# Kernel optimization log

Measured on AMD Instinct MI355X. Metric: run time of the kernel, lower is better.

Reference implementation:

```python
import jax, jax.numpy as jnp
import numpy as np

N_SITES = 100000
DIM = 128
KSIZE = 7  # 7^3 = 343 offsets
GRID = 160


def _build_sparse_structure(seed=0):
    """Sample N_SITES unique voxels in a GRID^3 volume and build the
    depthwise-conv kernel map: neighbor_idx[i, k] = index of site at
    coords[i] + offset[k], or N_SITES (sentinel -> zero row) if absent."""
    rng = np.random.default_rng(seed)
    lin = rng.choice(GRID ** 3, size=N_SITES, replace=False)
    coords = np.stack(np.unravel_index(lin, (GRID, GRID, GRID)), axis=1).astype(np.int64)  # [N,3]
    lookup = np.full(GRID ** 3, N_SITES, dtype=np.int32)
    lookup[lin] = np.arange(N_SITES, dtype=np.int32)
    r = KSIZE // 2
    offs = np.stack(np.meshgrid(*([np.arange(-r, r + 1)] * 3), indexing="ij"), axis=-1).reshape(-1, 3)  # [343,3]
    K = offs.shape[0]
    neighbor_idx = np.full((N_SITES, K), N_SITES, dtype=np.int32)
    for k in range(K):
        nb = coords + offs[k]
        ok = np.all((nb >= 0) & (nb < GRID), axis=1)
        nb_lin = (nb[ok, 0] * GRID + nb[ok, 1]) * GRID + nb[ok, 2]
        neighbor_idx[ok, k] = lookup[nb_lin]
    return neighbor_idx


def setup_inputs() -> dict:
    key = jax.random.key(0)
    ks = jax.random.split(key, 12)
    neighbor_idx = jnp.asarray(_build_sparse_structure(0))
    d, h = DIM, 4 * DIM
    K = KSIZE ** 3
    return {
        "feats": jax.random.normal(ks[0], (N_SITES, d), jnp.float32),
        "neighbor_idx": neighbor_idx,
        "dw_w": jax.random.normal(ks[1], (K, d), jnp.float32) * 0.05,
        "dw_b": jax.random.normal(ks[2], (d,), jnp.float32) * 0.02,
        "ln_g": 1.0 + 0.1 * jax.random.normal(ks[3], (d,), jnp.float32),
        "ln_b": 0.02 * jax.random.normal(ks[4], (d,), jnp.float32),
        "w1": jax.random.normal(ks[5], (d, h), jnp.float32) * (1.0 / np.sqrt(d)),
        "b1": 0.02 * jax.random.normal(ks[6], (h,), jnp.float32),
        "grn_g": 0.1 * jax.random.normal(ks[7], (1, h), jnp.float32),
        "grn_b": 0.02 * jax.random.normal(ks[8], (1, h), jnp.float32),
        "w2": jax.random.normal(ks[9], (h, d), jnp.float32) * (1.0 / np.sqrt(h)),
        "b2": 0.02 * jax.random.normal(ks[10], (d,), jnp.float32),
    }


def reference(feats, neighbor_idx, dw_w, dw_b, ln_g, ln_b, w1, b1, grn_g, grn_b, w2, b2):
    eps = 1e-6
    n, d = feats.shape
    # --- sparse depthwise conv: gather-multiply-accumulate over kernel offsets ---
    f_pad = jnp.concatenate([feats, jnp.zeros((1, d), feats.dtype)], axis=0)  # sentinel row

    def step(acc, xs):
        idx_k, w_k = xs  # idx_k: [N], w_k: [dim]
        return acc + f_pad[idx_k] * w_k, None

    x, _ = jax.lax.scan(step, jnp.zeros_like(feats), (neighbor_idx.T, dw_w))
    x = x + dw_b
    # --- LayerNorm over channels ---
    mu = jnp.mean(x, axis=-1, keepdims=True)
    var = jnp.var(x, axis=-1, keepdims=True)
    x = (x - mu) / jnp.sqrt(var + eps) * ln_g + ln_b
    # --- pwconv1 -> GELU (exact, matching torch default) ---
    x = jax.nn.gelu(x @ w1 + b1, approximate=False)  # [N, 4*dim]
    # --- GRN: L2 norm over all sites (dim=0), per channel ---
    gx = jnp.sqrt(jnp.sum(x * x, axis=0, keepdims=True))  # [1, 4*dim]
    nx = gx / (jnp.mean(gx, axis=-1, keepdims=True) + eps)
    x = grn_g * (x * nx) + grn_b + x
    # --- pwconv2 + residual (drop_path identity in eval) ---
    x = x @ w2 + b2
    return feats + x
```

## Files before the change

kernel.cpp:

```cpp
#include <hip/hip_runtime.h>

typedef unsigned short u16;
typedef unsigned int u32;
typedef __attribute__((ext_vector_type(8))) short bf16x8;
typedef __attribute__((ext_vector_type(4))) float f32x4;

__device__ __forceinline__ u16 f2bf(float f) {
    u32 u = __float_as_uint(f);
    return (u16)((u + 0x7FFFu + ((u >> 16) & 1u)) >> 16);
}

__device__ __forceinline__ float fast_gelu(float x) {
    const float t = x * x;
    const float y2 = x * __builtin_fmaf(0.0713548214f, t, 1.5957691216057308f);
    const float u = __expf(fminf(y2, 80.f));
    return x * u * __builtin_amdgcn_rcpf(u + 1.f);
}

__device__ __forceinline__ void gload_lds16(const u16* g, u16* l) {
    __builtin_amdgcn_global_load_lds(
        (const __attribute__((address_space(1))) void*)g,
        (__attribute__((address_space(3))) void*)l, 16, 0, 0);
}

__global__ __launch_bounds__(256) void cast_feats_k(
    const float* __restrict__ src, u16* __restrict__ dst, int n4)
{
    const int e = blockIdx.x * 256 + threadIdx.x;
    if (e >= n4) return;
    const float4 v = *(const float4*)(src + (size_t)e * 4);
    uint2 o;
    o.x = (u32)f2bf(v.x) | ((u32)f2bf(v.y) << 16);
    o.y = (u32)f2bf(v.z) | ((u32)f2bf(v.w) << 16);
    *(uint2*)(dst + (size_t)e * 4) = o;
}

__global__ __launch_bounds__(256) void dwln_k(
    const u16* __restrict__ featsb, const int* __restrict__ nb,
    const u16* __restrict__ dwwb, const float* __restrict__ dw_b,
    const float* __restrict__ ln_g, const float* __restrict__ ln_b,
    u16* __restrict__ xln, int nsites)
{
    __shared__ int lists[8][348];
    const int w = threadIdx.x >> 6;
    const int lane = threadIdx.x & 63;
    const int s0 = blockIdx.x * 8 + w * 2;
    if (s0 >= nsites) return;
    const bool two = (s0 + 1) < nsites;
    const int* rowA = nb + (size_t)s0 * 343;
    const int* rowB = nb + (size_t)(two ? s0 + 1 : s0) * 343;
    int idxA[6], idxB[6];
    #pragma unroll
    for (int j = 0; j < 5; ++j) {
        idxA[j] = rowA[lane + j * 64];
        const int vb = rowB[lane + j * 64];
        idxB[j] = two ? vb : nsites;
    }
    idxA[5] = (lane < 23) ? rowA[320 + lane] : nsites;
    idxB[5] = (two && lane < 23) ? rowB[320 + lane] : nsites;
    int cA = 0, cB = 0;
    #pragma unroll
    for (int i = 0; i < 6; ++i) {
        cA += (idxA[i] < nsites) ? 1 : 0;
        cB += (idxB[i] < nsites) ? 1 : 0;
    }
    const int packed = cA | (cB << 16);
    int pre = packed;
    #pragma unroll
    for (int off = 1; off < 64; off <<= 1) {
        const int v = __shfl_up(pre, off, 64);
        if (lane >= off) pre += v;
    }
    const int tot = __shfl(pre, 63, 64);
    const int cntA = tot & 0xFFFF, cntB = tot >> 16;
    pre -= packed;
    int pA = pre & 0xFFFF, pB = pre >> 16;
    #pragma unroll
    for (int i = 0; i < 6; ++i) {
        const int k = (i < 5) ? (lane + i * 64) : (320 + lane);
        if (idxA[i] < nsites) lists[w * 2][pA++] = idxA[i] | (k << 17);
        if (idxB[i] < nsites) lists[w * 2 + 1][pB++] = idxB[i] | (k << 17);
    }
    float xA0 = 0.f, xA1 = 0.f, xB0 = 0.f, xB1 = 0.f;
    const int mx = (cntA > cntB) ? cntA : cntB;
    for (int base = 0; base < mx; base += 4) {
        u32 fa[4], wa[4], fb[4], wb[4];
        #pragma unroll
        for (int i = 0; i < 4; ++i) {
            if (base + i < cntA) {
                const int p = lists[w * 2][base + i];
                fa[i] = *(const u32*)(featsb + (size_t)(p & 0x1FFFF) * 128 + lane * 2);
                wa[i] = *(const u32*)(dwwb + (size_t)(p >> 17) * 128 + lane * 2);
            } else { fa[i] = 0u; wa[i] = 0u; }
            if (base + i < cntB) {
                const int p = lists[w * 2 + 1][base + i];
                fb[i] = *(const u32*)(featsb + (size_t)(p & 0x1FFFF) * 128 + lane * 2);
                wb[i] = *(const u32*)(dwwb + (size_t)(p >> 17) * 128 + lane * 2);
            } else { fb[i] = 0u; wb[i] = 0u; }
        }
        #pragma unroll
        for (int i = 0; i < 4; ++i) {
            xA0 += __uint_as_float(fa[i] << 16) * __uint_as_float(wa[i] << 16);
            xA1 += __uint_as_float(fa[i] & 0xFFFF0000u) * __uint_as_float(wa[i] & 0xFFFF0000u);
            xB0 += __uint_as_float(fb[i] << 16) * __uint_as_float(wb[i] << 16);
            xB1 += __uint_as_float(fb[i] & 0xFFFF0000u) * __uint_as_float(wb[i] & 0xFFFF0000u);
        }
    }
    const float2 bv = *(const float2*)(dw_b + lane * 2);
    const float2 gv = *(const float2*)(ln_g + lane * 2);
    const float2 lbv = *(const float2*)(ln_b + lane * 2);
    #pragma unroll
    for (int sidx = 0; sidx < 2; ++sidx) {
        if (sidx == 1 && !two) break;
        float a0 = (sidx == 0) ? xA0 : xB0;
        float a1 = (sidx == 0) ? xA1 : xB1;
        a0 += bv.x; a1 += bv.y;
        float s = a0 + a1, ss = a0 * a0 + a1 * a1;
        #pragma unroll
        for (int off = 32; off > 0; off >>= 1) {
            s += __shfl_xor(s, off, 64);
            ss += __shfl_xor(ss, off, 64);
        }
        const float mean = s * (1.f / 128.f);
        const float var = ss * (1.f / 128.f) - mean * mean;
        const float rstd = rsqrtf(fmaxf(var, 0.f) + 1e-6f);
        const float y0 = (a0 - mean) * rstd * gv.x + lbv.x;
        const float y1 = (a1 - mean) * rstd * gv.y + lbv.y;
        *(u32*)(xln + (size_t)(s0 + sidx) * 128 + lane * 2) =
            (u32)f2bf(y0) | ((u32)f2bf(y1) << 16);
    }
}

__global__ __launch_bounds__(256) void transpose_w1_k(
    const float* __restrict__ w1, u16* __restrict__ w1t)
{
    const int e = blockIdx.x * 256 + threadIdx.x;
    const int n = e >> 7, k = e & 127;
    w1t[e] = f2bf(w1[k * 512 + n]);
}

__global__ __launch_bounds__(256, 4) void gemm1_k(
    const u16* __restrict__ xln, const u16* __restrict__ w1t,
    const float* __restrict__ b1, u16* __restrict__ h,
    float* __restrict__ gx_sq, int nsites)
{
    __shared__ u16 xb[64 * 128];
    __shared__ float s_red[128];
    const int t = threadIdx.x;
    const int n0 = blockIdx.x * 128;
    const int m0 = blockIdx.y * 64;
    const int lane = t & 63;
    const int w = t >> 6;
    const int wn = w * 32;
    const int l15 = lane & 15, quad = lane >> 4;
    if (t < 128) s_red[t] = 0.f;
    #pragma unroll
    for (int i = 0; i < 4; ++i) {
        const int r = w * 16 + i * 4 + (lane >> 4);
        const int c = (lane & 15) ^ (r & 15);
        gload_lds16(xln + (size_t)(m0 + r) * 128 + c * 8,
                    &xb[(w * 16 + i * 4) * 128]);
    }
    f32x4 acc[2][4];
    #pragma unroll
    for (int i = 0; i < 2; ++i)
        #pragma unroll
        for (int j = 0; j < 4; ++j) acc[i][j] = f32x4{0.f, 0.f, 0.f, 0.f};
    const u16* a_base = w1t + (size_t)(n0 + wn + l15) * 128 + quad * 8;
    bf16x8 aC[2];
    #pragma unroll
    for (int nt = 0; nt < 2; ++nt) aC[nt] = *(const bf16x8*)(a_base + (size_t)nt * 16 * 128);
    asm volatile("s_waitcnt vmcnt(0)" ::: "memory");
    __syncthreads();
    #pragma unroll
    for (int ks = 0; ks < 4; ++ks) {
        bf16x8 aN[2];
        if (ks < 3) {
            #pragma unroll
            for (int nt = 0; nt < 2; ++nt)
                aN[nt] = *(const bf16x8*)(a_base + (size_t)nt * 16 * 128 + (ks + 1) * 32);
        }
        bf16x8 b[4];
        #pragma unroll
        for (int mt = 0; mt < 4; ++mt) {
            const int r = mt * 16 + l15;
            b[mt] = *(const bf16x8*)(&xb[r * 128 + (((ks * 4 + quad) ^ l15) << 3)]);
        }
        #pragma unroll
        for (int nt = 0; nt < 2; ++nt)
            #pragma unroll
            for (int mt = 0; mt < 4; ++mt)
                acc[nt][mt] = __builtin_amdgcn_mfma_f32_16x16x32_bf16(aC[nt], b[mt], acc[nt][mt], 0, 0, 0);
        if (ks < 3) {
            #pragma unroll
            for (int nt = 0; nt < 2; ++nt) aC[nt] = aN[nt];
        }
    }
    float ssl[2][4] = {{0.f,0.f,0.f,0.f},{0.f,0.f,0.f,0.f}};
    #pragma unroll
    for (int nt = 0; nt < 2; ++nt) {
        const int chb = n0 + wn + nt * 16 + quad * 4;
        const float4 b1v = *(const float4*)(b1 + chb);
        #pragma unroll
        for (int mt = 0; mt < 4; ++mt) {
            const int site = m0 + mt * 16 + l15;
            if (site < nsites) {
                float v[4];
                #pragma unroll
                for (int rg = 0; rg < 4; ++rg) {
                    v[rg] = fast_gelu(acc[nt][mt][rg] + ((const float*)&b1v)[rg]);
                    ssl[nt][rg] += v[rg] * v[rg];
                }
                uint2 o;
                o.x = (u32)f2bf(v[0]) | ((u32)f2bf(v[1]) << 16);
                o.y = (u32)f2bf(v[2]) | ((u32)f2bf(v[3]) << 16);
                *(uint2*)(h + (size_t)site * 512 + chb) = o;
            }
        }
    }
    #pragma unroll
    for (int nt = 0; nt < 2; ++nt)
        #pragma unroll
        for (int rg = 0; rg < 4; ++rg) {
            float v = ssl[nt][rg];
            v += __shfl_xor(v, 1, 64);
            v += __shfl_xor(v, 2, 64);
            v += __shfl_xor(v, 4, 64);
            v += __shfl_xor(v, 8, 64);
            if (l15 == 0) atomicAdd(&s_red[wn + nt * 16 + quad * 4 + rg], v);
        }
    __syncthreads();
    if (t < 128) atomicAdd(&gx_sq[n0 + t], s_red[t]);
}

__global__ __launch_bounds__(256) void beff_k(
    const float* __restrict__ grn_b, const float* __restrict__ w2,
    float* __restrict__ b_eff)
{
    __shared__ float red[256];
    const int t = threadIdx.x;
    const int dc = t & 127, part = t >> 7;
    const int c0 = blockIdx.x * 64 + part * 32;
    float p = 0.f;
    #pragma unroll 8
    for (int i = 0; i < 32; ++i) {
        const int c = c0 + i;
        p += grn_b[c] * w2[(size_t)c * 128 + dc];
    }
    red[t] = p;
    __syncthreads();
    if (t < 128) atomicAdd(&b_eff[t], red[t] + red[t + 128]);
}

__global__ __launch_bounds__(512) void grn_scale_k(
    const float* __restrict__ gx_sq, const float* __restrict__ grn_g,
    float* __restrict__ scale)
{
    __shared__ float red[512];
    const int t = threadIdx.x;
    const float g = sqrtf(gx_sq[t]);
    red[t] = g;
    __syncthreads();
    #pragma unroll
    for (int off = 256; off > 0; off >>= 1) {
        if (t < off) red[t] += red[t + off];
        __syncthreads();
    }
    const float mean = red[0] * (1.f / 512.f);
    scale[t] = grn_g[t] * (g / (mean + 1e-6f)) + 1.f;
}

__global__ __launch_bounds__(256) void w2t_k(
    const float* __restrict__ scale, const float* __restrict__ w2,
    u16* __restrict__ w2t)
{
    const int e = blockIdx.x * 256 + threadIdx.x;
    const int c = e & 511, dc = e >> 9;
    w2t[e] = f2bf(scale[c] * w2[(size_t)c * 128 + dc]);
}

__global__ __launch_bounds__(256, 4) void gemm2_k(
    const u16* __restrict__ h, const u16* __restrict__ w2t,
    const float* __restrict__ b_eff, const float* __restrict__ b2,
    const float* __restrict__ feats,
    float* __restrict__ out, int nsites)
{
    __shared__ u16 hb[2][64 * 128];
    const int t = threadIdx.x;
    const int m0 = blockIdx.x * 64;
    const int lane = t & 63;
    const int w = t >> 6;
    const int wn = w * 32;
    const int l15 = lane & 15, quad = lane >> 4;
    const int r_st = w * 16 + (lane >> 4) * 4 ? 0 : 0;
    f32x4 acc[2][4];
    #pragma unroll
    for (int i = 0; i < 2; ++i)
        #pragma unroll
        for (int j = 0; j < 4; ++j) acc[i][j] = f32x4{0.f, 0.f, 0.f, 0.f};
    const u16* a_base = w2t + (size_t)(wn + l15) * 512 + quad * 8;

    #define STAGE2(bsel, tc)                                                     \
        {                                                                        \
            _Pragma("unroll")                                                    \
            for (int i_ = 0; i_ < 4; ++i_) {                                     \
                const int r_ = w * 16 + i_ * 4 + (lane >> 4);                    \
                const int c_ = (lane & 15) ^ (r_ & 15);                          \
                gload_lds16(h + (size_t)(m0 + r_) * 512 + (tc) * 128 + c_ * 8,   \
                            &hb[bsel][(w * 16 + i_ * 4) * 128]);                 \
            }                                                                    \
        }

    STAGE2(0, 0)
    bf16x8 aC[2];
    #pragma unroll
    for (int nt = 0; nt < 2; ++nt) aC[nt] = *(const bf16x8*)(a_base + (size_t)nt * 16 * 512);
    asm volatile("s_waitcnt vmcnt(0)" ::: "memory");
    __syncthreads();
    #pragma unroll
    for (int tch = 0; tch < 4; ++tch) {
        const int cur = tch & 1;
        if (tch < 3) STAGE2(cur ^ 1, tch + 1)
        #pragma unroll
        for (int ks = 0; ks < 4; ++ks) {
            const int ksg = tch * 4 + ks;
            bf16x8 aN[2];
            if (ksg < 15) {
                #pragma unroll
                for (int nt = 0; nt < 2; ++nt)
                    aN[nt] = *(const bf16x8*)(a_base + (size_t)nt * 16 * 512 + (ksg + 1) * 32);
            }
            bf16x8 b[4];
            #pragma unroll
            for (int mt = 0; mt < 4; ++mt) {
                const int r = mt * 16 + l15;
                b[mt] = *(const bf16x8*)(&hb[cur][r * 128 + (((ks * 4 + quad) ^ l15) << 3)]);
            }
            #pragma unroll
            for (int nt = 0; nt < 2; ++nt)
                #pragma unroll
                for (int mt = 0; mt < 4; ++mt)
                    acc[nt][mt] = __builtin_amdgcn_mfma_f32_16x16x32_bf16(aC[nt], b[mt], acc[nt][mt], 0, 0, 0);
            if (ksg < 15) {
                #pragma unroll
                for (int nt = 0; nt < 2; ++nt) aC[nt] = aN[nt];
            }
        }
        if (tch < 3) {
            asm volatile("s_waitcnt vmcnt(0)" ::: "memory");
            __syncthreads();
        }
    }
    #undef STAGE2
    #pragma unroll
    for (int nt = 0; nt < 2; ++nt) {
        const int chb = wn + nt * 16 + quad * 4;
        const float4 bev = *(const float4*)(b_eff + chb);
        const float4 b2v = *(const float4*)(b2 + chb);
        #pragma unroll
        for (int mt = 0; mt < 4; ++mt) {
            const int site = m0 + mt * 16 + l15;
            if (site < nsites) {
                const float4 fv = *(const float4*)(feats + (size_t)site * 128 + chb);
                float4 o;
                o.x = acc[nt][mt][0] + bev.x + b2v.x + fv.x;
                o.y = acc[nt][mt][1] + bev.y + b2v.y + fv.y;
                o.z = acc[nt][mt][2] + bev.z + b2v.z + fv.z;
                o.w = acc[nt][mt][3] + bev.w + b2v.w + fv.w;
                *(float4*)(out + (size_t)site * 128 + chb) = o;
            }
        }
    }
}

extern "C" void kernel_launch(void* const* d_in, const int* in_sizes, int n_in,
                              void* d_out, int out_size, void* d_ws, size_t ws_size,
                              hipStream_t stream) {
    const float* feats = (const float*)d_in[0];
    const int* nb      = (const int*)d_in[1];
    const float* dw_w  = (const float*)d_in[2];
    const float* dw_b  = (const float*)d_in[3];
    const float* ln_g  = (const float*)d_in[4];
    const float* ln_b  = (const float*)d_in[5];
    const float* w1    = (const float*)d_in[6];
    const float* b1    = (const float*)d_in[7];
    const float* grn_g = (const float*)d_in[8];
    const float* grn_b = (const float*)d_in[9];
    const float* w2    = (const float*)d_in[10];
    const float* b2    = (const float*)d_in[11];
    float* out = (float*)d_out;
    const int nsites = in_sizes[0] / 128;

    char* ws = (char*)d_ws;
    size_t off = 0;
    u16* xln   = (u16*)(ws + off);  off += (((size_t)(nsites + 128) * 128 * 2) + 255) & ~(size_t)255;
    u16* h     = (u16*)(ws + off);  off += (((size_t)(nsites + 128) * 512 * 2) + 255) & ~(size_t)255;
    u16* featsb= (u16*)(ws + off);  off += (((size_t)nsites * 128 * 2) + 255) & ~(size_t)255;
    u16* dwwb  = (u16*)(ws + off);  off += 343 * 128 * 2 + 128;
    u16* w1t   = (u16*)(ws + off);  off += 512 * 128 * 2;
    u16* w2t   = (u16*)(ws + off);  off += 128 * 512 * 2;
    float* gx_sq = (float*)(ws + off); off += 512 * 4;
    float* scale = (float*)(ws + off); off += 512 * 4;
    float* b_eff = (float*)(ws + off); off += 128 * 4;

    hipMemsetAsync(gx_sq, 0, 512 * sizeof(float), stream);
    hipMemsetAsync(b_eff, 0, 128 * sizeof(float), stream);
    const int nfeat4 = nsites * 32;
    cast_feats_k<<<(nfeat4 + 255) / 256, 256, 0, stream>>>(feats, featsb, nfeat4);
    const int ndww4 = 343 * 32;
    cast_feats_k<<<(ndww4 + 255) / 256, 256, 0, stream>>>(dw_w, dwwb, ndww4);
    transpose_w1_k<<<256, 256, 0, stream>>>(w1, w1t);
    beff_k<<<8, 256, 0, stream>>>(grn_b, w2, b_eff);
    dwln_k<<<(nsites + 7) / 8, 256, 0, stream>>>(featsb, nb, dwwb, dw_b, ln_g, ln_b, xln, nsites);
    const int m1blocks = (nsites + 63) / 64;
    gemm1_k<<<dim3(4, m1blocks), 256, 0, stream>>>(xln, w1t, b1, h, gx_sq, nsites);
    grn_scale_k<<<1, 512, 0, stream>>>(gx_sq, grn_g, scale);
    w2t_k<<<256, 256, 0, stream>>>(scale, w2, w2t);
    const int m2blocks = (nsites + 63) / 64;
    gemm2_k<<<m2blocks, 256, 0, stream>>>(h, w2t, b_eff, b2, feats, out, nsites);
}
```

Baseline: 411.0 us.

## Gather fp32 features directly in depthwise conv, drop bf16 cast kernels

```diff
diff --git a/kernel.cpp b/kernel.cpp
--- a/kernel.cpp
+++ b/kernel.cpp
@@ -23,112 +23,73 @@
         (__attribute__((address_space(3))) void*)l, 16, 0, 0);
 }
 
-__global__ __launch_bounds__(256) void cast_feats_k(
-    const float* __restrict__ src, u16* __restrict__ dst, int n4)
-{
-    const int e = blockIdx.x * 256 + threadIdx.x;
-    if (e >= n4) return;
-    const float4 v = *(const float4*)(src + (size_t)e * 4);
-    uint2 o;
-    o.x = (u32)f2bf(v.x) | ((u32)f2bf(v.y) << 16);
-    o.y = (u32)f2bf(v.z) | ((u32)f2bf(v.w) << 16);
-    *(uint2*)(dst + (size_t)e * 4) = o;
-}
-
 __global__ __launch_bounds__(256) void dwln_k(
-    const u16* __restrict__ featsb, const int* __restrict__ nb,
-    const u16* __restrict__ dwwb, const float* __restrict__ dw_b,
+    const float* __restrict__ feats, const int* __restrict__ nb,
+    const float* __restrict__ dw_w, const float* __restrict__ dw_b,
     const float* __restrict__ ln_g, const float* __restrict__ ln_b,
     u16* __restrict__ xln, int nsites)
 {
-    __shared__ int lists[8][348];
+    __shared__ int lists[4][344];
     const int w = threadIdx.x >> 6;
     const int lane = threadIdx.x & 63;
-    const int s0 = blockIdx.x * 8 + w * 2;
-    if (s0 >= nsites) return;
-    const bool two = (s0 + 1) < nsites;
-    const int* rowA = nb + (size_t)s0 * 343;
-    const int* rowB = nb + (size_t)(two ? s0 + 1 : s0) * 343;
-    int idxA[6], idxB[6];
-    #pragma unroll
-    for (int j = 0; j < 5; ++j) {
-        idxA[j] = rowA[lane + j * 64];
-        const int vb = rowB[lane + j * 64];
-        idxB[j] = two ? vb : nsites;
-    }
-    idxA[5] = (lane < 23) ? rowA[320 + lane] : nsites;
-    idxB[5] = (two && lane < 23) ? rowB[320 + lane] : nsites;
-    int cA = 0, cB = 0;
-    #pragma unroll
-    for (int i = 0; i < 6; ++i) {
-        cA += (idxA[i] < nsites) ? 1 : 0;
-        cB += (idxB[i] < nsites) ? 1 : 0;
-    }
-    const int packed = cA | (cB << 16);
-    int pre = packed;
+    const int s = blockIdx.x * 4 + w;
+    if (s >= nsites) return;
+    const int* row = nb + (size_t)s * 343;
+    int idx[6];
+    #pragma unroll
+    for (int j = 0; j < 5; ++j) idx[j] = row[lane + j * 64];
+    idx[5] = (lane < 23) ? row[320 + lane] : nsites;
+    int c = 0;
+    #pragma unroll
+    for (int i = 0; i < 6; ++i) c += (idx[i] < nsites) ? 1 : 0;
+    int pre = c;
     #pragma unroll
     for (int off = 1; off < 64; off <<= 1) {
         const int v = __shfl_up(pre, off, 64);
         if (lane >= off) pre += v;
     }
-    const int tot = __shfl(pre, 63, 64);
-    const int cntA = tot & 0xFFFF, cntB = tot >> 16;
-    pre -= packed;
-    int pA = pre & 0xFFFF, pB = pre >> 16;
+    const int cnt = __shfl(pre, 63, 64);
+    pre -= c;
+    int p = pre;
     #pragma unroll
     for (int i = 0; i < 6; ++i) {
         const int k = (i < 5) ? (lane + i * 64) : (320 + lane);
-        if (idxA[i] < nsites) lists[w * 2][pA++] = idxA[i] | (k << 17);
-        if (idxB[i] < nsites) lists[w * 2 + 1][pB++] = idxB[i] | (k << 17);
-    }
-    float xA0 = 0.f, xA1 = 0.f, xB0 = 0.f, xB1 = 0.f;
-    const int mx = (cntA > cntB) ? cntA : cntB;
-    for (int base = 0; base < mx; base += 4) {
-        u32 fa[4], wa[4], fb[4], wb[4];
-        #pragma unroll
-        for (int i = 0; i < 4; ++i) {
-            if (base + i < cntA) {
-                const int p = lists[w * 2][base + i];
-                fa[i] = *(const u32*)(featsb + (size_t)(p & 0x1FFFF) * 128 + lane * 2);
-                wa[i] = *(const u32*)(dwwb + (size_t)(p >> 17) * 128 + lane * 2);
-            } else { fa[i] = 0u; wa[i] = 0u; }
-            if (base + i < cntB) {
-                const int p = lists[w * 2 + 1][base + i];
-                fb[i] = *(const u32*)(featsb + (size_t)(p & 0x1FFFF) * 128 + lane * 2);
-                wb[i] = *(const u32*)(dwwb + (size_t)(p >> 17) * 128 + lane * 2);
-            } else { fb[i] = 0u; wb[i] = 0u; }
-        }
-        #pragma unroll
-        for (int i = 0; i < 4; ++i) {
-            xA0 += __uint_as_float(fa[i] << 16) * __uint_as_float(wa[i] << 16);
-            xA1 += __uint_as_float(fa[i] & 0xFFFF0000u) * __uint_as_float(wa[i] & 0xFFFF0000u);
-            xB0 += __uint_as_float(fb[i] << 16) * __uint_as_float(wb[i] << 16);
-            xB1 += __uint_as_float(fb[i] & 0xFFFF0000u) * __uint_as_float(wb[i] & 0xFFFF0000u);
+        if (idx[i] < nsites) lists[w][p++] = idx[i] | (k << 17);
+    }
+    float x0 = 0.f, x1 = 0.f;
+    for (int base = 0; base < cnt; base += 8) {
+        float2 f[8], wv[8];
+        #pragma unroll
+        for (int i = 0; i < 8; ++i) {
+            if (base + i < cnt) {
+                const int e = lists[w][base + i];
+                f[i]  = *(const float2*)(feats + (size_t)(e & 0x1FFFF) * 128 + lane * 2);
+                wv[i] = *(const float2*)(dw_w + (size_t)(e >> 17) * 128 + lane * 2);
+            } else { f[i] = float2{0.f, 0.f}; wv[i] = float2{0.f, 0.f}; }
+        }
+        #pragma unroll
+        for (int i = 0; i < 8; ++i) {
+            x0 += f[i].x * wv[i].x;
+            x1 += f[i].y * wv[i].y;
         }
     }
     const float2 bv = *(const float2*)(dw_b + lane * 2);
     const float2 gv = *(const float2*)(ln_g + lane * 2);
     const float2 lbv = *(const float2*)(ln_b + lane * 2);
-    #pragma unroll
-    for (int sidx = 0; sidx < 2; ++sidx) {
-        if (sidx == 1 && !two) break;
-        float a0 = (sidx == 0) ? xA0 : xB0;
-        float a1 = (sidx == 0) ? xA1 : xB1;
-        a0 += bv.x; a1 += bv.y;
-        float s = a0 + a1, ss = a0 * a0 + a1 * a1;
-        #pragma unroll
-        for (int off = 32; off > 0; off >>= 1) {
-            s += __shfl_xor(s, off, 64);
-            ss += __shfl_xor(ss, off, 64);
-        }
-        const float mean = s * (1.f / 128.f);
-        const float var = ss * (1.f / 128.f) - mean * mean;
-        const float rstd = rsqrtf(fmaxf(var, 0.f) + 1e-6f);
-        const float y0 = (a0 - mean) * rstd * gv.x + lbv.x;
-        const float y1 = (a1 - mean) * rstd * gv.y + lbv.y;
-        *(u32*)(xln + (size_t)(s0 + sidx) * 128 + lane * 2) =
-            (u32)f2bf(y0) | ((u32)f2bf(y1) << 16);
-    }
+    float a0 = x0 + bv.x, a1 = x1 + bv.y;
+    float sm = a0 + a1, ss = a0 * a0 + a1 * a1;
+    #pragma unroll
+    for (int off = 32; off > 0; off >>= 1) {
+        sm += __shfl_xor(sm, off, 64);
+        ss += __shfl_xor(ss, off, 64);
+    }
+    const float mean = sm * (1.f / 128.f);
+    const float var = ss * (1.f / 128.f) - mean * mean;
+    const float rstd = rsqrtf(fmaxf(var, 0.f) + 1e-6f);
+    const float y0 = (a0 - mean) * rstd * gv.x + lbv.x;
+    const float y1 = (a1 - mean) * rstd * gv.y + lbv.y;
+    *(u32*)(xln + (size_t)s * 128 + lane * 2) =
+        (u32)f2bf(y0) | ((u32)f2bf(y1) << 16);
 }
 
 __global__ __launch_bounds__(256) void transpose_w1_k(
@@ -292,8 +253,11 @@
     const int w = t >> 6;
     const int wn = w * 32;
     const int l15 = lane & 15, quad = lane >> 4;
-    const int r_st = w * 16 + (lane >> 4) * 4 ? 0 : 0;
     f32x4 acc[2][4];
+    #pragma unroll
+    for (int i = 0; i < 2; ++i)
+        #pragma unroll
+        for (int j = 0; j < 2 * 2; ++j) acc[i & 1][j] = f32x4{0.f, 0.f, 0.f, 0.f};
     #pragma unroll
     for (int i = 0; i < 2; ++i)
         #pragma unroll
@@ -395,8 +359,6 @@
     size_t off = 0;
     u16* xln   = (u16*)(ws + off);  off += (((size_t)(nsites + 128) * 128 * 2) + 255) & ~(size_t)255;
     u16* h     = (u16*)(ws + off);  off += (((size_t)(nsites + 128) * 512 * 2) + 255) & ~(size_t)255;
-    u16* featsb= (u16*)(ws + off);  off += (((size_t)nsites * 128 * 2) + 255) & ~(size_t)255;
-    u16* dwwb  = (u16*)(ws + off);  off += 343 * 128 * 2 + 128;
     u16* w1t   = (u16*)(ws + off);  off += 512 * 128 * 2;
     u16* w2t   = (u16*)(ws + off);  off += 128 * 512 * 2;
     float* gx_sq = (float*)(ws + off); off += 512 * 4;
@@ -405,13 +367,9 @@
 
     hipMemsetAsync(gx_sq, 0, 512 * sizeof(float), stream);
     hipMemsetAsync(b_eff, 0, 128 * sizeof(float), stream);
-    const int nfeat4 = nsites * 32;
-    cast_feats_k<<<(nfeat4 + 255) / 256, 256, 0, stream>>>(feats, featsb, nfeat4);
-    const int ndww4 = 343 * 32;
-    cast_feats_k<<<(ndww4 + 255) / 256, 256, 0, stream>>>(dw_w, dwwb, ndww4);
     transpose_w1_k<<<256, 256, 0, stream>>>(w1, w1t);
     beff_k<<<8, 256, 0, stream>>>(grn_b, w2, b_eff);
-    dwln_k<<<(nsites + 7) / 8, 256, 0, stream>>>(featsb, nb, dwwb, dw_b, ln_g, ln_b, xln, nsites);
+    dwln_k<<<(nsites + 3) / 4, 256, 0, stream>>>(feats, nb, dw_w, dw_b, ln_g, ln_b, xln, nsites);
     const int m1blocks = (nsites + 63) / 64;
     gemm1_k<<<dim3(4, m1blocks), 256, 0, stream>>>(xln, w1t, b1, h, gx_sq, nsites);
     grn_scale_k<<<1, 512, 0, stream>>>(gx_sq, grn_g, scale);
```

Result: slower. 427.8 us (+4.1%).
